# Kernel tuning notes

Measured on AMD Instinct MI355X. Metric: run time of the kernel, lower is better.

## Reference

```python
import jax, jax.numpy as jnp
import numpy as np

B, N, NF, C = 1, 5000, 10000, 128   # batch, vertices, faces, feature width
LAYERS = 30
NNZ = 48 * B * NF  # ~3 verts/face * 16 entries per 4x4 quaternion block


def spmm(rows, cols, vals, x, n_rows):
    # sparse COO [n_rows, n_cols] @ dense x [n_cols, d] -> [n_rows, d]
    return jax.ops.segment_sum(vals[:, None] * x[cols], rows, num_segments=n_rows)


def graph_bn(x, gamma, beta, eps=1e-5):
    # GraphBatchNorm: BatchNorm1d over (batch, nodes) per channel, training-mode stats
    mean = jnp.mean(x, axis=(0, 1))
    var = jnp.var(x, axis=(0, 1))
    return gamma * (x - mean) * jax.lax.rsqrt(var + eps) + beta


def gc_pre(x, gamma, beta, W, b):
    # GraphConv1x1 with batch_norm='pre'
    return graph_bn(x, gamma, beta) @ W + b


def _forward(inputs, mask, Di_rows, Di_cols, Di_vals, DiA_rows, DiA_cols, DiA_vals,
             W_in, b_in, g0, be0, W0, b0, g1, be1, Wl1, bl1, g2, be2, W_out, b_out):
    Bv, Nv, _ = inputs.shape
    v = inputs @ W_in + b_in                      # conv1 (batch_norm=None)
    f = jnp.zeros((Bv, NF, C), inputs.dtype)      # face features start at zero
    for i in range(LAYERS):
        if i % 2 == 0:
            # DirResNet2: Dirac operator message passing vertices<->faces
            x_in, f_in = jax.nn.elu(v), jax.nn.elu(f)
            # vertices -> faces; C channels viewed as 4 quaternion components x C//4
            Dv = spmm(Di_rows, Di_cols, Di_vals,
                      x_in.reshape(Bv * Nv * 4, C // 4), 4 * Bv * NF).reshape(Bv, NF, C)
            f_out = gc_pre(jnp.concatenate([f_in, Dv], -1), g0[i], be0[i], W0[i], b0[i])
            # adjoint Dirac: faces -> vertices
            DAf = spmm(DiA_rows, DiA_cols, DiA_vals,
                       jax.nn.elu(f_out).reshape(Bv * NF * 4, C // 4), 4 * Bv * Nv).reshape(Bv, Nv, C)
            v = v + gc_pre(jnp.concatenate([x_in, DAf], -1), g1[i], be1[i], Wl1[i], bl1[i])
            f = f_out
        else:
            # AvgResNet2: masked global average pooling block
            x = v
            for (g, be, W, b) in ((g0[i], be0[i], W0[i], b0[i]),
                                  (g1[i], be1[i], Wl1[i], bl1[i])):
                x = jax.nn.elu(x)
                avg = jnp.sum(x * mask, axis=1, keepdims=True) / jnp.sum(mask, axis=1, keepdims=True)
                x = jnp.concatenate([x, jnp.broadcast_to(avg, x.shape)], -1)
                x = gc_pre(x, g, be, W, b)
            v = x + v
    out = gc_pre(v, g2, be2, W_out, b_out)        # conv2 (batch_norm='pre')
    return jax.nn.elu(out)


def setup_inputs():
    key = jax.random.key(0)
    ks = jax.random.split(key, 12)
    return {
        "inputs": jax.random.normal(ks[0], (B, N, 3), jnp.float32),
        "mask": jnp.ones((B, N, 1), jnp.float32),
        "Di_rows": jax.random.randint(ks[1], (NNZ,), 0, 4 * B * NF, jnp.int32),
        "Di_cols": jax.random.randint(ks[2], (NNZ,), 0, 4 * B * N, jnp.int32),
        "Di_vals": jax.random.normal(ks[3], (NNZ,), jnp.float32),
        "DiA_rows": jax.random.randint(ks[4], (NNZ,), 0, 4 * B * N, jnp.int32),
        "DiA_cols": jax.random.randint(ks[5], (NNZ,), 0, 4 * B * NF, jnp.int32),
        "DiA_vals": jax.random.normal(ks[6], (NNZ,), jnp.float32),
        "W_in": jax.random.normal(ks[7], (3, C), jnp.float32) * 0.5,
        "b_in": jnp.zeros((C,), jnp.float32),
        "g0": jnp.ones((LAYERS, 2 * C), jnp.float32),
        "be0": jnp.zeros((LAYERS, 2 * C), jnp.float32),
        "W0": jax.random.normal(ks[8], (LAYERS, 2 * C, C), jnp.float32) * 0.05,
        "b0": jnp.zeros((LAYERS, C), jnp.float32),
        "g1": jnp.ones((LAYERS, 2 * C), jnp.float32),
        "be1": jnp.zeros((LAYERS, 2 * C), jnp.float32),
        "Wl1": jax.random.normal(ks[9], (LAYERS, 2 * C, C), jnp.float32) * 0.05,
        "bl1": jnp.zeros((LAYERS, C), jnp.float32),
        "g2": jnp.ones((C,), jnp.float32),
        "be2": jnp.zeros((C,), jnp.float32),
        "W_out": jax.random.normal(ks[10], (C, 1), jnp.float32) * 0.1,
        "b_out": jnp.zeros((1,), jnp.float32),
    }


def reference(inputs, mask, Di_rows, Di_cols, Di_vals, DiA_rows, DiA_cols, DiA_vals,
              W_in, b_in, g0, be0, W0, b0, g1, be1, Wl1, bl1, g2, be2, W_out, b_out):
    return _forward(inputs, mask, Di_rows, Di_cols, Di_vals, DiA_rows, DiA_cols, DiA_vals,
                    W_in, b_in, g0, be0, W0, b0, g1, be1, Wl1, bl1, g2, be2, W_out, b_out)
```

## Files before the change

kernel.cpp:

```cpp
#include <hip/hip_runtime.h>
#include <math.h>

#define N_V 5000
#define N_F 10000
#define NNZ 480000
#define LAYERS 30
#define STC 4096

typedef short short8 __attribute__((ext_vector_type(8)));
typedef float f32x4 __attribute__((ext_vector_type(4)));
union BFu { uint4 u; short8 s8; short s[8]; unsigned short us[8]; };

__device__ __forceinline__ float eluf(float x){ return x>0.f ? x : expm1f(x); }
__device__ __forceinline__ unsigned short f2bf(float f){
  unsigned u = __float_as_uint(f);
  unsigned r = (u + 0x7fffu + ((u>>16)&1u)) >> 16;
  return (unsigned short)r;
}
__device__ __forceinline__ float bf2f(unsigned short u){
  return __uint_as_float((unsigned)u << 16);
}

__global__ void hist_both(const int* __restrict__ Di_rows, const int* __restrict__ DiA_rows,
                          int* __restrict__ Di_cur, int* __restrict__ DA_cur){
  int e = blockIdx.x*256 + threadIdx.x;
  if(e < NNZ){
    atomicAdd(&Di_cur[Di_rows[e]], 1);
    atomicAdd(&DA_cur[DiA_rows[e]], 1);
  }
}

__global__ void chunkscan(const int* __restrict__ Di_cur, int* __restrict__ Di_ptr,
                          const int* __restrict__ DA_cur, int* __restrict__ DA_ptr,
                          int* __restrict__ bsumDi, int* __restrict__ bsumDA){
  __shared__ int ish[256];
  int b = blockIdx.x, tid = threadIdx.x;
  const int nchDi = 157;
  const int* hist; int* optr; int n; int cb; int* bs;
  if(b < nchDi){ hist=Di_cur; optr=Di_ptr; n=40000; cb=b; bs=bsumDi; }
  else { hist=DA_cur; optr=DA_ptr; n=20000; cb=b-nchDi; bs=bsumDA; }
  int i = cb*256 + tid;
  int v = (i<n)? hist[i] : 0;
  ish[tid]=v; __syncthreads();
  for(int off=1; off<256; off<<=1){
    int t = (tid>=off)? ish[tid-off] : 0;
    __syncthreads(); ish[tid]+=t; __syncthreads();
  }
  if(i<n) optr[i] = ish[tid]-v;
  if(tid==255) bs[cb]=ish[255];
}

__global__ void topscan(int* __restrict__ bsumDi, int* __restrict__ bsumDA){
  __shared__ int ish[256];
  int tid=threadIdx.x;
  int* bs = (blockIdx.x==0) ? bsumDi : bsumDA;
  int n  = (blockIdx.x==0) ? 157 : 79;
  int v = (tid<n)? bs[tid] : 0;
  ish[tid]=v; __syncthreads();
  for(int off=1; off<256; off<<=1){
    int t=(tid>=off)? ish[tid-off]:0;
    __syncthreads(); ish[tid]+=t; __syncthreads();
  }
  if(tid<n) bs[tid]=ish[tid]-v;
}

__global__ void addback(int* __restrict__ Di_ptr, int* __restrict__ Di_cur,
                        const int* __restrict__ bsumDi,
                        int* __restrict__ DA_ptr, int* __restrict__ DA_cur,
                        const int* __restrict__ bsumDA){
  int stride = gridDim.x*256;
  int base = blockIdx.x*256 + threadIdx.x;
  for(int i=base;i<40000;i+=stride){ int v=Di_ptr[i]+bsumDi[i>>8]; Di_ptr[i]=v; Di_cur[i]=v; }
  for(int i=base;i<20000;i+=stride){ int v=DA_ptr[i]+bsumDA[i>>8]; DA_ptr[i]=v; DA_cur[i]=v; }
  if(base==0){ Di_ptr[40000]=NNZ; DA_ptr[20000]=NNZ; }
}

__global__ void scatter_pairs(const int* __restrict__ Di_rows, int* __restrict__ Di_cur,
                              const int* __restrict__ Di_cols, const float* __restrict__ Di_vals,
                              float2* __restrict__ Di_pairs,
                              const int* __restrict__ DiA_rows, int* __restrict__ DA_cur,
                              const int* __restrict__ DiA_cols, const float* __restrict__ DiA_vals,
                              float2* __restrict__ DA_pairs){
  int g = blockIdx.x & 7;
  int sub = blockIdx.x >> 3;
  int lo_di = g*5000, hi_di = lo_di+5000;
  int lo_da = g*2500, hi_da = lo_da+2500;
  int stride = (gridDim.x>>3)*256;
  for(int e = sub*256 + threadIdx.x; e < NNZ; e += stride){
    int r = Di_rows[e];
    if(r >= lo_di && r < hi_di){
      int pos = atomicAdd(&Di_cur[r], 1);
      Di_pairs[pos] = make_float2(__int_as_float(Di_cols[e]), Di_vals[e]);
    }
    r = DiA_rows[e];
    if(r >= lo_da && r < hi_da){
      int pos = atomicAdd(&DA_cur[r], 1);
      DA_pairs[pos] = make_float2(__int_as_float(DiA_cols[e]), DiA_vals[e]);
    }
  }
}

__global__ void wconv(const float* __restrict__ W0, const float* __restrict__ Wl1,
                      unsigned short* __restrict__ Wt){
  __shared__ float tile[32][129];
  int b  = blockIdx.x >> 3;
  int kt = blockIdx.x & 7;
  int i = b>>1, m = b&1;
  const float* W = (m ? Wl1 : W0) + (size_t)i*32768;
  unsigned short* out = Wt + (size_t)b*32768;
  int tid = threadIdx.x;
  int n = tid & 127, kr = tid >> 7;
  for(int kk = kr; kk < 32; kk += 2)
    tile[kk][n] = W[(kt*32 + kk)*128 + n];
  __syncthreads();
  int kp = tid & 31, n8 = tid >> 5;
  for(int nn = n8; nn < 128; nn += 8)
    out[nn*256 + kt*32 + kp] = f2bf(tile[kp][nn]);
}

__global__ void conv1_kernel(const float* __restrict__ in, const float* __restrict__ W_in,
                             const float* __restrict__ b_in,
                             const float* __restrict__ be0, const float* __restrict__ W0,
                             const float* __restrict__ be1, const float* __restrict__ Wl1,
                             float* __restrict__ v_raw, unsigned short* __restrict__ elu_v,
                             float* __restrict__ st1, float* __restrict__ oddb){
  __shared__ float pool[256];
  int tid = threadIdx.x;
  int stride = gridDim.x*256;
  int cpy = (blockIdx.x&7)*512;
  float ls=0.f, ls2=0.f;
  for(int idx = blockIdx.x*256+tid; idx < N_V*128; idx += stride){
    int n = idx>>7, c = idx&127;
    float v = b_in[c] + in[n*3]*W_in[c] + in[n*3+1]*W_in[128+c] + in[n*3+2]*W_in[256+c];
    v_raw[idx] = v;
    float ev = eluf(v);
    elu_v[idx] = f2bf(ev);
    ls += ev; ls2 += ev*ev;
  }
  int ch = tid & 127;
  pool[tid]=ls; __syncthreads();
  if(tid<128) atomicAdd(&st1[cpy+ch], pool[tid]+pool[tid+128]);
  __syncthreads();
  pool[tid]=ls2; __syncthreads();
  if(tid<128) atomicAdd(&st1[cpy+256+ch], pool[tid]+pool[tid+128]);
  for(int item = blockIdx.x*256+tid; item < LAYERS*2*128; item += stride){
    int i = item >> 8;
    int m = (item >> 7) & 1;
    int j = item & 127;
    const float* be = m ? be1 : be0;
    const float* W  = m ? Wl1 : W0;
    const float* wp = W + (size_t)i*32768 + 128*128 + j;
    const float* bp = be + i*256 + 128;
    float s = 0.f;
    for(int k=0;k<128;++k) s += bp[k]*wp[k*128];
    oddb[item] = s;
  }
}

__global__ __launch_bounds__(256) void spmm_bn(
    const int* __restrict__ ptr, const float2* __restrict__ pairs,
    const unsigned short* __restrict__ x, float* __restrict__ y, int nrows,
    float* __restrict__ stslot){
  __shared__ float pool[512];
  int tid = threadIdx.x;
  int w = tid>>6, lane = tid&63;
  int slot = lane>>3, jg = lane&7;
  int row = blockIdx.x*32 + w*8 + slot;
  float4 acc = make_float4(0,0,0,0);
  if(row < nrows){
    int s0 = ptr[row], e0 = ptr[row+1];
    int last = e0 - 1;
    for(int i = s0; i < e0; i += 4){
      int i1 = min(i+1, last), i2 = min(i+2, last), i3 = min(i+3, last);
      float2 p0 = pairs[i];
      float2 p1 = pairs[i1];
      float2 p2 = pairs[i2];
      float2 p3 = pairs[i3];
      float w1 = (i+1 <= last) ? p1.y : 0.f;
      float w2 = (i+2 <= last) ? p2.y : 0.f;
      float w3 = (i+3 <= last) ? p3.y : 0.f;
      ushort4 x0 = *(const ushort4*)&x[(__float_as_int(p0.x)<<5) + jg*4];
      ushort4 x1 = *(const ushort4*)&x[(__float_as_int(p1.x)<<5) + jg*4];
      ushort4 x2 = *(const ushort4*)&x[(__float_as_int(p2.x)<<5) + jg*4];
      ushort4 x3 = *(const ushort4*)&x[(__float_as_int(p3.x)<<5) + jg*4];
      acc.x += p0.y*bf2f(x0.x) + w1*bf2f(x1.x) + w2*bf2f(x2.x) + w3*bf2f(x3.x);
      acc.y += p0.y*bf2f(x0.y) + w1*bf2f(x1.y) + w2*bf2f(x2.y) + w3*bf2f(x3.y);
      acc.z += p0.y*bf2f(x0.z) + w1*bf2f(x1.z) + w2*bf2f(x2.z) + w3*bf2f(x3.z);
      acc.w += p0.y*bf2f(x0.w) + w1*bf2f(x1.w) + w2*bf2f(x2.w) + w3*bf2f(x3.w);
    }
    *(float4*)&y[(row<<5) + jg*4] = acc;
  }
  float4 ls2 = make_float4(acc.x*acc.x, acc.y*acc.y, acc.z*acc.z, acc.w*acc.w);
  acc.x += __shfl_xor(acc.x, 32); acc.y += __shfl_xor(acc.y, 32);
  acc.z += __shfl_xor(acc.z, 32); acc.w += __shfl_xor(acc.w, 32);
  ls2.x += __shfl_xor(ls2.x, 32); ls2.y += __shfl_xor(ls2.y, 32);
  ls2.z += __shfl_xor(ls2.z, 32); ls2.w += __shfl_xor(ls2.w, 32);
  if(slot < 4) *(float4*)&pool[w*128 + slot*32 + jg*4] = acc;
  __syncthreads();
  int cpy = (blockIdx.x&7)*512;
  if(tid < 128){
    int c = (tid + (blockIdx.x<<3)) & 127;
    atomicAdd(&stslot[cpy+128+c], pool[c]+pool[128+c]+pool[256+c]+pool[384+c]);
  }
  __syncthreads();
  if(slot < 4) *(float4*)&pool[w*128 + slot*32 + jg*4] = ls2;
  __syncthreads();
  if(tid < 128){
    int c = (tid + (blockIdx.x<<3)) & 127;
    atomicAdd(&stslot[cpy+384+c], pool[c]+pool[128+c]+pool[256+c]+pool[384+c]);
  }
}

__global__ __launch_bounds__(256) void gemm_mfma(
    const unsigned short* __restrict__ A0, const float* __restrict__ A1,
    const float* __restrict__ st, float invM,
    const float* __restrict__ g, const float* __restrict__ be,
    const unsigned short* __restrict__ Wt, const float* __restrict__ bias,
    const float* __restrict__ bias2, const float* __restrict__ resid,
    float* __restrict__ out_raw, unsigned short* __restrict__ out_elu,
    float* __restrict__ stE, float* __restrict__ stR, int M, int K)
{
  __shared__ float ab[256], bb[256];
  int tid = threadIdx.x;
  if(tid < K){
    float s1 = 0.f, s2v = 0.f;
    #pragma unroll
    for(int c8=0;c8<8;++c8){ s1 += st[c8*512 + tid]; s2v += st[c8*512 + 256 + tid]; }
    float mean = s1*invM;
    float var  = fmaxf(s2v*invM - mean*mean, 0.f);
    float aa   = g[tid]*rsqrtf(var + 1e-5f);
    ab[tid] = aa; bb[tid] = be[tid] - mean*aa;
  }
  __syncthreads();

  int wave = tid>>6, lane = tid&63;
  int ln = lane&15, q = lane>>4;
  int r0 = blockIdx.x*16;
  int c0 = wave*32;
  int kq = q*8;
  int arow = r0 + ln;
  bool aok = arow < M;

  f32x4 acc[2] = {};
  for(int kb=0; kb<K; kb+=32){
    int kg = kb + kq;
    float av[8];
    if(!aok){
      #pragma unroll
      for(int j2=0;j2<8;++j2) av[j2]=0.f;
    } else if(A1 && kg >= 128){
      int kk = kg - 128;
      float4 x0 = *(const float4*)&A1[arow*128 + kk];
      float4 x1 = *(const float4*)&A1[arow*128 + kk + 4];
      av[0]=x0.x; av[1]=x0.y; av[2]=x0.z; av[3]=x0.w;
      av[4]=x1.x; av[5]=x1.y; av[6]=x1.z; av[7]=x1.w;
    } else {
      BFu raw; raw.u = *(const uint4*)&A0[arow*128 + kg];
      #pragma unroll
      for(int j2=0;j2<8;++j2) av[j2] = bf2f(raw.us[j2]);
    }
    BFu af;
    #pragma unroll
    for(int j2=0;j2<8;++j2) af.us[j2] = f2bf(fmaf(av[j2], ab[kg+j2], bb[kg+j2]));
    #pragma unroll
    for(int nb=0;nb<2;++nb){
      int n = c0 + nb*16 + ln;
      BFu bfv; bfv.u = *(const uint4*)&Wt[n*256 + kb + kq];
      acc[nb] = __builtin_amdgcn_mfma_f32_16x16x32_bf16(af.s8, bfv.s8, acc[nb], 0, 0, 0);
    }
  }

  __syncthreads();

  int rbase = r0 + q*4;
  bool wantR = (stR != nullptr);
  int cpy = (blockIdx.x&7)*512;
  #pragma unroll
  for(int nb=0;nb<2;++nb){
    int col = c0 + nb*16 + ln;
    float bsum = bias[col] + (bias2 ? bias2[col] : 0.f);
    float s=0.f, s2=0.f, rs=0.f, rs2=0.f;
    #pragma unroll
    for(int reg=0;reg<4;++reg){
      int row = rbase + reg;
      bool ok = row < M;
      float v = acc[nb][reg] + bsum;
      if(resid && ok) v += resid[row*128 + col];
      float ve = eluf(v);
      if(ok){
        if(out_raw) out_raw[row*128 + col] = v;
        if(out_elu) out_elu[row*128 + col] = f2bf(ve);
        s += ve; s2 += ve*ve;
        if(wantR){ rs += v; rs2 += v*v; }
      }
    }
    s  += __shfl_xor(s, 16);  s  += __shfl_xor(s, 32);
    s2 += __shfl_xor(s2, 16); s2 += __shfl_xor(s2, 32);
    if(wantR){
      rs  += __shfl_xor(rs, 16);  rs  += __shfl_xor(rs, 32);
      rs2 += __shfl_xor(rs2, 16); rs2 += __shfl_xor(rs2, 32);
    }
    if(q==0){
      if(stE){ atomicAdd(&stE[cpy+col], s); atomicAdd(&stE[cpy+256+col], s2); }
      if(wantR){ atomicAdd(&stR[cpy+col], rs); atomicAdd(&stR[cpy+256+col], rs2); }
    }
  }
}

__global__ void final_kernel(const float* __restrict__ v_raw, const float* __restrict__ st,
                             const float* __restrict__ g2, const float* __restrict__ be2,
                             const float* __restrict__ W_out, const float* __restrict__ b_out,
                             float* __restrict__ out){
  __shared__ float pool[256];
  int tid = threadIdx.x; int half = tid>>7, k = tid&127;
  float s1 = 0.f, s2v = 0.f;
  #pragma unroll
  for(int c8=0;c8<8;++c8){ s1 += st[c8*512 + k]; s2v += st[c8*512 + 256 + k]; }
  float mean = s1*(1.f/N_V);
  float var = fmaxf(s2v*(1.f/N_V) - mean*mean, 0.f);
  float aa = g2[k]*rsqrtf(var+1e-5f);
  float scale = aa*W_out[k];
  float cons = (be2[k]-mean*aa)*W_out[k];
  int r = blockIdx.x*2 + half;
  float val = v_raw[r*128+k]*scale + cons;
  pool[tid]=val; __syncthreads();
  for(int s=64;s>=1;s>>=1){ if(k<s) pool[tid]+=pool[tid+s]; __syncthreads(); }
  if(k==0) out[r] = eluf(pool[tid] + b_out[0]);
}

extern "C" void kernel_launch(void* const* d_in, const int* in_sizes, int n_in,
                              void* d_out, int out_size, void* d_ws, size_t ws_size,
                              hipStream_t stream){
  const float* inputs  = (const float*)d_in[0];
  const int*   Di_rows = (const int*)d_in[2];
  const int*   Di_cols = (const int*)d_in[3];
  const float* Di_vals = (const float*)d_in[4];
  const int*   DiA_rows= (const int*)d_in[5];
  const int*   DiA_cols= (const int*)d_in[6];
  const float* DiA_vals= (const float*)d_in[7];
  const float* W_in = (const float*)d_in[8];  const float* b_in = (const float*)d_in[9];
  const float* g0  = (const float*)d_in[10];  const float* be0 = (const float*)d_in[11];
  const float* W0  = (const float*)d_in[12];  const float* b0  = (const float*)d_in[13];
  const float* g1  = (const float*)d_in[14];  const float* be1 = (const float*)d_in[15];
  const float* Wl1 = (const float*)d_in[16];  const float* bl1 = (const float*)d_in[17];
  const float* g2  = (const float*)d_in[18];  const float* be2 = (const float*)d_in[19];
  const float* W_out = (const float*)d_in[20]; const float* b_out = (const float*)d_in[21];

  float* ws = (float*)d_ws;
  float* v_raw = ws;
  unsigned short* elu_v = (unsigned short*)(ws + 640000);
  unsigned short* elu_f = (unsigned short*)(ws + 1280000);
  float* Dv    = ws + 2560000;
  float* DAf   = ws + 3840000;
  float* st    = ws + 4480000;
  float* oddb  = ws + 4742144;
  int* Di_ptr  = (int*)(ws + 4749824);
  int* DA_ptr  = (int*)(ws + 4789825);
  int* Di_cur  = (int*)(ws + 4809826);
  int* DA_cur  = (int*)(ws + 4849826);
  float2* Di_pairs = (float2*)(ws + 4869826);
  float2* DA_pairs = (float2*)(ws + 5829826);
  int* bsumDi  = (int*)(ws + 6789826);
  int* bsumDA  = (int*)(ws + 6790082);
  unsigned short* Wt = (unsigned short*)(ws + 6790210);
  unsigned short* elu_x1 = (unsigned short*)Dv;

  hipMemsetAsync(st, 0, (size_t)64*STC*sizeof(float), stream);
  hipMemsetAsync(elu_f, 0, (size_t)1280000*sizeof(unsigned short), stream);
  hipMemsetAsync(Di_cur, 0, (size_t)60000*sizeof(int), stream);

  hist_both<<<1875, 256, 0, stream>>>(Di_rows, DiA_rows, Di_cur, DA_cur);
  chunkscan<<<236, 256, 0, stream>>>(Di_cur, Di_ptr, DA_cur, DA_ptr, bsumDi, bsumDA);
  topscan<<<2, 256, 0, stream>>>(bsumDi, bsumDA);
  addback<<<236, 256, 0, stream>>>(Di_ptr, Di_cur, bsumDi, DA_ptr, DA_cur, bsumDA);
  scatter_pairs<<<2048, 256, 0, stream>>>(Di_rows, Di_cur, Di_cols, Di_vals, Di_pairs,
                                          DiA_rows, DA_cur, DiA_cols, DiA_vals, DA_pairs);
  wconv<<<480, 256, 0, stream>>>(W0, Wl1, Wt);
  conv1_kernel<<<640, 256, 0, stream>>>(inputs, W_in, b_in, be0, W0, be1, Wl1,
                                        v_raw, elu_v, st + STC, oddb);

  for(int i=0;i<LAYERS;++i){
    if((i&1)==0){
      float* S0  = st + (size_t)(2*i)*STC;
      float* S1b = st + (size_t)(2*i+1)*STC;
      spmm_bn<<<1250, 256, 0, stream>>>(Di_ptr, Di_pairs, elu_v, Dv, 40000, S0);
      gemm_mfma<<<625, 256, 0, stream>>>(elu_f, Dv, S0, 1.f/N_F, g0+i*256, be0+i*256,
                                         Wt + (size_t)(2*i)*32768, b0+i*128, nullptr,
                                         nullptr, nullptr, elu_f,
                                         st+(size_t)(2*(i+2))*STC, nullptr, N_F, 256);
      spmm_bn<<<625, 256, 0, stream>>>(DA_ptr, DA_pairs, elu_f, DAf, 20000, S1b);
      gemm_mfma<<<313, 256, 0, stream>>>(elu_v, DAf, S1b, 1.f/N_V, g1+i*256, be1+i*256,
                                         Wt + (size_t)(2*i+1)*32768, bl1+i*128, nullptr,
                                         v_raw, v_raw, elu_v,
                                         st+(size_t)(2*(i+1))*STC, nullptr, N_V, 256);
    } else {
      float* S0  = st + (size_t)(2*i)*STC;
      float* S1b = st + (size_t)(2*i+1)*STC;
      gemm_mfma<<<313, 256, 0, stream>>>(elu_v, nullptr, S0, 1.f/N_V, g0+i*256, be0+i*256,
                                         Wt + (size_t)(2*i)*32768, b0+i*128, oddb+i*256,
                                         nullptr, nullptr, elu_x1,
                                         S1b, nullptr, N_V, 128);
      float* stE = (i==LAYERS-1) ? nullptr : st+(size_t)(2*i+3)*STC;
      float* stR = (i==LAYERS-1) ? st+(size_t)62*STC : nullptr;
      gemm_mfma<<<313, 256, 0, stream>>>(elu_x1, nullptr, S1b, 1.f/N_V, g1+i*256, be1+i*256,
                                         Wt + (size_t)(2*i+1)*32768, bl1+i*128, oddb+i*256+128,
                                         v_raw, v_raw, elu_v,
                                         stE, stR, N_V, 128);
    }
  }
  final_kernel<<<2500, 256, 0, stream>>>(v_raw, st+(size_t)62*STC, g2, be2, W_out, b_out,
                                         (float*)d_out);
}
```

Before: 1.274 ms.

## Split GEMM into single-wave blocks with ping-pong activation buffers, unroll SpMM gathers

The GEMM kernel drops from four-wave 256-thread blocks to one-wave 64-thread blocks, each computing a 16x32 tile. The bf16 ELU activation buffers become double-buffered so a GEMM no longer reads and writes the same array in place, which lets the trailing __syncthreads be removed. SpMM now batches 8 gathers per iteration instead of 4 to keep more loads in flight. The odd-layer bias precompute reads bf16 transposed weights instead of fp32, which changes its rounding slightly. The cost is per-block BN-stat setup repeated across four times as many blocks, plus extra workspace.

```diff
diff --git a/kernel.cpp b/kernel.cpp
--- a/kernel.cpp
+++ b/kernel.cpp
@@ -120,8 +120,8 @@
 
 __global__ void conv1_kernel(const float* __restrict__ in, const float* __restrict__ W_in,
                              const float* __restrict__ b_in,
-                             const float* __restrict__ be0, const float* __restrict__ W0,
-                             const float* __restrict__ be1, const float* __restrict__ Wl1,
+                             const float* __restrict__ be0, const float* __restrict__ be1,
+                             const unsigned short* __restrict__ Wt,
                              float* __restrict__ v_raw, unsigned short* __restrict__ elu_v,
                              float* __restrict__ st1, float* __restrict__ oddb){
   __shared__ float pool[256];
@@ -144,15 +144,14 @@
   pool[tid]=ls2; __syncthreads();
   if(tid<128) atomicAdd(&st1[cpy+256+ch], pool[tid]+pool[tid+128]);
   for(int item = blockIdx.x*256+tid; item < LAYERS*2*128; item += stride){
-    int i = item >> 8;
-    int m = (item >> 7) & 1;
+    int b = item >> 7;
+    int i = b >> 1, m = b & 1;
     int j = item & 127;
-    const float* be = m ? be1 : be0;
-    const float* W  = m ? Wl1 : W0;
-    const float* wp = W + (size_t)i*32768 + 128*128 + j;
-    const float* bp = be + i*256 + 128;
+    const float* bp = (m ? be1 : be0) + i*256 + 128;
+    const unsigned short* wp = Wt + (size_t)b*32768 + j*256 + 128;
     float s = 0.f;
-    for(int k=0;k<128;++k) s += bp[k]*wp[k*128];
+    #pragma unroll 8
+    for(int k=0;k<128;++k) s += bp[k]*bf2f(wp[k]);
     oddb[item] = s;
   }
 }
@@ -170,23 +169,21 @@
   if(row < nrows){
     int s0 = ptr[row], e0 = ptr[row+1];
     int last = e0 - 1;
-    for(int i = s0; i < e0; i += 4){
-      int i1 = min(i+1, last), i2 = min(i+2, last), i3 = min(i+3, last);
-      float2 p0 = pairs[i];
-      float2 p1 = pairs[i1];
-      float2 p2 = pairs[i2];
-      float2 p3 = pairs[i3];
-      float w1 = (i+1 <= last) ? p1.y : 0.f;
-      float w2 = (i+2 <= last) ? p2.y : 0.f;
-      float w3 = (i+3 <= last) ? p3.y : 0.f;
-      ushort4 x0 = *(const ushort4*)&x[(__float_as_int(p0.x)<<5) + jg*4];
-      ushort4 x1 = *(const ushort4*)&x[(__float_as_int(p1.x)<<5) + jg*4];
-      ushort4 x2 = *(const ushort4*)&x[(__float_as_int(p2.x)<<5) + jg*4];
-      ushort4 x3 = *(const ushort4*)&x[(__float_as_int(p3.x)<<5) + jg*4];
-      acc.x += p0.y*bf2f(x0.x) + w1*bf2f(x1.x) + w2*bf2f(x2.x) + w3*bf2f(x3.x);
-      acc.y += p0.y*bf2f(x0.y) + w1*bf2f(x1.y) + w2*bf2f(x2.y) + w3*bf2f(x3.y);
-      acc.z += p0.y*bf2f(x0.z) + w1*bf2f(x1.z) + w2*bf2f(x2.z) + w3*bf2f(x3.z);
-      acc.w += p0.y*bf2f(x0.w) + w1*bf2f(x1.w) + w2*bf2f(x2.w) + w3*bf2f(x3.w);
+    for(int i = s0; i < e0; i += 8){
+      float2 p[8]; float wgt[8]; ushort4 xv[8];
+      #pragma unroll
+      for(int u=0;u<8;++u) p[u] = pairs[min(i+u, last)];
+      #pragma unroll
+      for(int u=0;u<8;++u) wgt[u] = (i+u <= last) ? p[u].y : 0.f;
+      #pragma unroll
+      for(int u=0;u<8;++u) xv[u] = *(const ushort4*)&x[(__float_as_int(p[u].x)<<5) + jg*4];
+      #pragma unroll
+      for(int u=0;u<8;++u){
+        acc.x += wgt[u]*bf2f(xv[u].x);
+        acc.y += wgt[u]*bf2f(xv[u].y);
+        acc.z += wgt[u]*bf2f(xv[u].z);
+        acc.w += wgt[u]*bf2f(xv[u].w);
+      }
     }
     *(float4*)&y[(row<<5) + jg*4] = acc;
   }
@@ -211,7 +208,7 @@
   }
 }
 
-__global__ __launch_bounds__(256) void gemm_mfma(
+__global__ __launch_bounds__(64) void gemm_mfma(
     const unsigned short* __restrict__ A0, const float* __restrict__ A1,
     const float* __restrict__ st, float invM,
     const float* __restrict__ g, const float* __restrict__ be,
@@ -222,21 +219,21 @@
 {
   __shared__ float ab[256], bb[256];
   int tid = threadIdx.x;
-  if(tid < K){
+  for(int c = tid; c < K; c += 64){
     float s1 = 0.f, s2v = 0.f;
     #pragma unroll
-    for(int c8=0;c8<8;++c8){ s1 += st[c8*512 + tid]; s2v += st[c8*512 + 256 + tid]; }
+    for(int c8=0;c8<8;++c8){ s1 += st[c8*512 + c]; s2v += st[c8*512 + 256 + c]; }
     float mean = s1*invM;
     float var  = fmaxf(s2v*invM - mean*mean, 0.f);
-    float aa   = g[tid]*rsqrtf(var + 1e-5f);
-    ab[tid] = aa; bb[tid] = be[tid] - mean*aa;
-  }
-  __syncthreads();
-
-  int wave = tid>>6, lane = tid&63;
+    float aa   = g[c]*rsqrtf(var + 1e-5f);
+    ab[c] = aa; bb[c] = be[c] - mean*aa;
+  }
+  __syncthreads();
+
+  int lane = tid;
   int ln = lane&15, q = lane>>4;
-  int r0 = blockIdx.x*16;
-  int c0 = wave*32;
+  int r0 = (blockIdx.x>>2)*16;
+  int c0 = (blockIdx.x&3)*32;
   int kq = q*8;
   int arow = r0 + ln;
   bool aok = arow < M;
@@ -269,8 +266,6 @@
       acc[nb] = __builtin_amdgcn_mfma_f32_16x16x32_bf16(af.s8, bfv.s8, acc[nb], 0, 0, 0);
     }
   }
-
-  __syncthreads();
 
   int rbase = r0 + q*4;
   bool wantR = (stR != nullptr);
@@ -348,8 +343,9 @@
 
   float* ws = (float*)d_ws;
   float* v_raw = ws;
-  unsigned short* elu_v = (unsigned short*)(ws + 640000);
-  unsigned short* elu_f = (unsigned short*)(ws + 1280000);
+  unsigned short* elu_v0 = (unsigned short*)(ws + 640000);
+  unsigned short* elu_v1 = (unsigned short*)(ws + 960000);
+  unsigned short* elu_f0 = (unsigned short*)(ws + 1280000);
   float* Dv    = ws + 2560000;
   float* DAf   = ws + 3840000;
   float* st    = ws + 4480000;
@@ -362,11 +358,15 @@
   float2* DA_pairs = (float2*)(ws + 5829826);
   int* bsumDi  = (int*)(ws + 6789826);
   int* bsumDA  = (int*)(ws + 6790082);
-  unsigned short* Wt = (unsigned short*)(ws + 6790210);
+  unsigned short* Wt = (unsigned short*)(ws + 6790212);
+  unsigned short* elu_f1 = (unsigned short*)(ws + 7773252);
   unsigned short* elu_x1 = (unsigned short*)Dv;
 
+  unsigned short* Vb[2] = {elu_v0, elu_v1};
+  unsigned short* Fb[2] = {elu_f0, elu_f1};
+
   hipMemsetAsync(st, 0, (size_t)64*STC*sizeof(float), stream);
-  hipMemsetAsync(elu_f, 0, (size_t)1280000*sizeof(unsigned short), stream);
+  hipMemsetAsync(elu_f0, 0, (size_t)1280000*sizeof(unsigned short), stream);
   hipMemsetAsync(Di_cur, 0, (size_t)60000*sizeof(int), stream);
 
   hist_both<<<1875, 256, 0, stream>>>(Di_rows, DiA_rows, Di_cur, DA_cur);
@@ -376,35 +376,38 @@
   scatter_pairs<<<2048, 256, 0, stream>>>(Di_rows, Di_cur, Di_cols, Di_vals, Di_pairs,
                                           DiA_rows, DA_cur, DiA_cols, DiA_vals, DA_pairs);
   wconv<<<480, 256, 0, stream>>>(W0, Wl1, Wt);
-  conv1_kernel<<<640, 256, 0, stream>>>(inputs, W_in, b_in, be0, W0, be1, Wl1,
-                                        v_raw, elu_v, st + STC, oddb);
-
+  conv1_kernel<<<640, 256, 0, stream>>>(inputs, W_in, b_in, be0, be1, Wt,
+                                        v_raw, elu_v0, st + STC, oddb);
+
+  int pv = 0, pf = 0;
   for(int i=0;i<LAYERS;++i){
     if((i&1)==0){
       float* S0  = st + (size_t)(2*i)*STC;
       float* S1b = st + (size_t)(2*i+1)*STC;
-      spmm_bn<<<1250, 256, 0, stream>>>(Di_ptr, Di_pairs, elu_v, Dv, 40000, S0);
-      gemm_mfma<<<625, 256, 0, stream>>>(elu_f, Dv, S0, 1.f/N_F, g0+i*256, be0+i*256,
+      spmm_bn<<<1250, 256, 0, stream>>>(Di_ptr, Di_pairs, Vb[pv], Dv, 40000, S0);
+      gemm_mfma<<<2500, 64, 0, stream>>>(Fb[pf], Dv, S0, 1.f/N_F, g0+i*256, be0+i*256,
                                          Wt + (size_t)(2*i)*32768, b0+i*128, nullptr,
-                                         nullptr, nullptr, elu_f,
+                                         nullptr, nullptr, Fb[pf^1],
                                          st+(size_t)(2*(i+2))*STC, nullptr, N_F, 256);
-      spmm_bn<<<625, 256, 0, stream>>>(DA_ptr, DA_pairs, elu_f, DAf, 20000, S1b);
-      gemm_mfma<<<313, 256, 0, stream>>>(elu_v, DAf, S1b, 1.f/N_V, g1+i*256, be1+i*256,
+      pf ^= 1;
+      spmm_bn<<<625, 256, 0, stream>>>(DA_ptr, DA_pairs, Fb[pf], DAf, 20000, S1b);
+      gemm_mfma<<<1252, 64, 0, stream>>>(Vb[pv], DAf, S1b, 1.f/N_V, g1+i*256, be1+i*256,
                                          Wt + (size_t)(2*i+1)*32768, bl1+i*128, nullptr,
-                                         v_raw, v_raw, elu_v,
+                                         v_raw, v_raw, Vb[pv^1],
                                          st+(size_t)(2*(i+1))*STC, nullptr, N_V, 256);
+      pv ^= 1;
     } else {
       float* S0  = st + (size_t)(2*i)*STC;
       float* S1b = st + (size_t)(2*i+1)*STC;
-      gemm_mfma<<<313, 256, 0, stream>>>(elu_v, nullptr, S0, 1.f/N_V, g0+i*256, be0+i*256,
+      gemm_mfma<<<1252, 64, 0, stream>>>(Vb[pv], nullptr, S0, 1.f/N_V, g0+i*256, be0+i*256,
                                          Wt + (size_t)(2*i)*32768, b0+i*128, oddb+i*256,
                                          nullptr, nullptr, elu_x1,
                                          S1b, nullptr, N_V, 128);
       float* stE = (i==LAYERS-1) ? nullptr : st+(size_t)(2*i+3)*STC;
       float* stR = (i==LAYERS-1) ? st+(size_t)62*STC : nullptr;
-      gemm_mfma<<<313, 256, 0, stream>>>(elu_x1, nullptr, S1b, 1.f/N_V, g1+i*256, be1+i*256,
+      gemm_mfma<<<1252, 64, 0, stream>>>(elu_x1, nullptr, S1b, 1.f/N_V, g1+i*256, be1+i*256,
                                          Wt + (size_t)(2*i+1)*32768, bl1+i*128, oddb+i*256+128,
-                                         v_raw, v_raw, elu_v,
+                                         v_raw, v_raw, Vb[pv],
                                          stE, stR, N_V, 128);
     }
   }
```

Result: slower. 1.405 ms (+10.3%).
